# Performance work log

Hardware: AMD Instinct MI355X
Metric: run time of the kernel (lower is better)

## Reference

```python
import jax, jax.numpy as jnp
import numpy as np

# bior3.5 analysis filters (pywt conventions, dec_len = 12).
# dec_lo derived from the CDF(3,5) construction: sqrt(2)/2048 * conv([1,5,10,10,5,1], [-20,160,-524,832,-524,160,-20])
# matches pywt: [-0.0138107, 0.0414420, 0.0524806, -0.2679272, -0.0718155, 0.9667476, ...] (symmetric)
_DEC_LO = jnp.asarray(
    np.array([-20., 60., 76., -388., -104., 1400., 1400., -104., -388., 76., 60., -20.]) * np.sqrt(2.0) / 2048.0,
    dtype=jnp.float32)
# dec_hi = QMF of rec_lo = sqrt(2)*[1,3,3,1]/8, zero-padded to length 12 as pywt stores it (phase matters for periodization)
_DEC_HI = jnp.asarray(
    np.array([0., 0., 0., 0., -1., 3., -3., 1., 0., 0., 0., 0.]) * np.sqrt(2.0) / 8.0,
    dtype=jnp.float32)


def _dwt_last(x, f):
    # pywt mode='periodization' along last axis: out[i] = sum_j f[j] * x[(2i+1-j) mod N], N even -> length N//2.
    # Equivalent to wrap-padding F-2 on the left, then stride-2 valid correlation with reversed filter.
    F = f.shape[0]
    N = x.shape[-1]
    xp = jnp.concatenate([x[..., N - (F - 2):], x], axis=-1)  # [..., N+F-2]
    lhs = xp.reshape(-1, 1, xp.shape[-1])
    rhs = f[::-1].astype(x.dtype).reshape(1, 1, F)
    out = jax.lax.conv_general_dilated(lhs, rhs, window_strides=(2,), padding='VALID')  # [M,1,N//2]
    return out.reshape(*x.shape[:-1], N // 2)


def _dwt_axis(x, f, axis):
    x = jnp.swapaxes(x, axis, -1)
    return jnp.swapaxes(_dwt_last(x, f), axis, -1)


def _dwt2(x):
    # separable 2D DWT over the last two axes; pywt dwt2 keys: 'aa','da','ad','dd' (first letter = axis -2)
    lo = _dwt_axis(x, _DEC_LO, -1)
    hi = _dwt_axis(x, _DEC_HI, -1)
    aa = _dwt_axis(lo, _DEC_LO, -2)  # cA
    da = _dwt_axis(lo, _DEC_HI, -2)  # cH
    ad = _dwt_axis(hi, _DEC_LO, -2)  # cV
    dd = _dwt_axis(hi, _DEC_HI, -2)  # cD
    return aa, (da, ad, dd)


def _forward(x, k):
    # wavedec2 to level k; the torch module stacks 3 channels (we carry them as a batch-like dim)
    # and concatenates (cH, cV, cD) along dim 0 for each level, coarsest level first.
    a = x
    highs = []
    for _ in range(k):
        a, (da, ad, dd) = _dwt2(a)
        highs.insert(0, jnp.concatenate([da, ad, dd], axis=0))  # [3B, 3, h, w]
    return (a, *highs)


def setup_inputs() -> dict:
    key = jax.random.key(0)
    x = jax.random.normal(key, (8, 3, 1024, 1024), dtype=jnp.float32)
    return {"x": x, "k": 3}


def reference(x, k):
    return _forward(x, k)
```

## Files before the change

kernel.cpp:

```cpp
#include <hip/hip_runtime.h>


#define OW 32
#define OHS 16
#define NSTEP 4
#define ROWS_PB (OHS * NSTEP)
#define IN_ROWS 42
#define QPR 20
#define NQ (IN_ROWS * QPR)
#define SPITCH 84
#define TRS 42

template <int N>
__global__ __launch_bounds__(256, 4) void dwt2_level(
    const float* __restrict__ src,
    float* __restrict__ aa, float* __restrict__ da,
    float* __restrict__ ad, float* __restrict__ dd)
{
    constexpr float SQ2 = 1.41421356237309504880f;
    constexpr float c_lo[12] = {
        -20.f * SQ2 / 2048.f,  60.f * SQ2 / 2048.f,   76.f * SQ2 / 2048.f,
        -388.f * SQ2 / 2048.f, -104.f * SQ2 / 2048.f, 1400.f * SQ2 / 2048.f,
        1400.f * SQ2 / 2048.f, -104.f * SQ2 / 2048.f, -388.f * SQ2 / 2048.f,
        76.f * SQ2 / 2048.f,   60.f * SQ2 / 2048.f,   -20.f * SQ2 / 2048.f };
    constexpr float c_hi4[4] = { -SQ2 / 8.f, 3.f * SQ2 / 8.f, -3.f * SQ2 / 8.f, SQ2 / 8.f };

    constexpr int h    = N >> 1;
    constexpr int mask = N - 1;

    const int bc  = blockIdx.z;
    const int j0  = blockIdx.x * OW;
    const int i0  = blockIdx.y * ROWS_PB;
    const int tid = threadIdx.x;

    __shared__ float s_in[IN_ROWS * SPITCH];
    __shared__ float s_loT[OW * TRS];
    __shared__ float s_hiT[OW * TRS];

    const float* img = src + (unsigned)bc * (unsigned)(N * N);
    const int c0 = 2 * j0 - 12;

    auto ldq = [&](int s, int q) -> float4 {
        const int r  = q / QPR;
        const int c4 = q - r * QPR;
        const int gr = (2 * (i0 + OHS * s) - 10 + r) & mask;
        const int gc = (c0 + 4 * c4) & mask;
        return *(const float4*)(img + (unsigned)(gr * N + gc));
    };
    auto stq = [&](int q, float4 v) {
        const int r  = q / QPR;
        const int c4 = q - r * QPR;
        *(float4*)&s_in[r * SPITCH + 4 * c4] = v;
    };

    const bool has4 = tid < (NQ - 768);

    float4 pf0 = ldq(0, tid);
    float4 pf1 = ldq(0, tid + 256);
    float4 pf2 = ldq(0, tid + 512);
    float4 pf3 = make_float4(0.f, 0.f, 0.f, 0.f);
    if (has4) pf3 = ldq(0, tid + 768);
    stq(tid, pf0);
    stq(tid + 256, pf1);
    stq(tid + 512, pf2);
    if (has4) stq(tid + 768, pf3);

    for (int s = 0; s < NSTEP; ++s) {
        __syncthreads();

        if (s + 1 < NSTEP) {
            pf0 = ldq(s + 1, tid);
            pf1 = ldq(s + 1, tid + 256);
            pf2 = ldq(s + 1, tid + 512);
            if (has4) pf3 = ldq(s + 1, tid + 768);
        }

        if (tid < IN_ROWS * (OW / 8)) {
            const int m = tid & 3;
            const int r = tid >> 2;
            const float* p = &s_in[r * SPITCH + 16 * m];
            float v[28];
            #pragma unroll
            for (int q = 0; q < 7; ++q)
                *(float4*)&v[4 * q] = *(const float4*)&p[4 * q];
            #pragma unroll
            for (int d = 0; d < 8; ++d) {
                float lo = 0.f, hi = 0.f;
                #pragma unroll
                for (int jc = 0; jc < 12; ++jc)
                    lo += c_lo[jc] * v[2 * d + 13 - jc];
                #pragma unroll
                for (int k = 0; k < 4; ++k)
                    hi += c_hi4[k] * v[2 * d + 9 - k];
                s_loT[(8 * m + d) * TRS + r] = lo;
                s_hiT[(8 * m + d) * TRS + r] = hi;
            }
        }
        __syncthreads();

        {
            const int tx = tid & 31;
            const int ty = tid >> 5;
            float l[14], hh[14];
            #pragma unroll
            for (int e = 0; e < 7; ++e) {
                *(float2*)&l[2 * e]  = *(const float2*)&s_loT[tx * TRS + 4 * ty + 2 * e];
                *(float2*)&hh[2 * e] = *(const float2*)&s_hiT[tx * TRS + 4 * ty + 2 * e];
            }
            float vaa0 = 0.f, vaa1 = 0.f, vad0 = 0.f, vad1 = 0.f;
            #pragma unroll
            for (int jr = 0; jr < 12; ++jr) {
                vaa0 += c_lo[jr] * l[11 - jr];
                vaa1 += c_lo[jr] * l[13 - jr];
                vad0 += c_lo[jr] * hh[11 - jr];
                vad1 += c_lo[jr] * hh[13 - jr];
            }
            float vda0 = 0.f, vda1 = 0.f, vdd0 = 0.f, vdd1 = 0.f;
            #pragma unroll
            for (int k = 0; k < 4; ++k) {
                vda0 += c_hi4[k] * l[7 - k];
                vda1 += c_hi4[k] * l[9 - k];
                vdd0 += c_hi4[k] * hh[7 - k];
                vdd1 += c_hi4[k] * hh[9 - k];
            }
            const int orow = i0 + OHS * s + 2 * ty;
            const unsigned ob = (unsigned)((bc * h + orow) * h + j0 + tx);
            aa[ob] = vaa0;  aa[ob + h] = vaa1;
            da[ob] = vda0;  da[ob + h] = vda1;
            ad[ob] = vad0;  ad[ob + h] = vad1;
            dd[ob] = vdd0;  dd[ob + h] = vdd1;
        }

        if (s + 1 < NSTEP) {
            stq(tid, pf0);
            stq(tid + 256, pf1);
            stq(tid + 512, pf2);
            if (has4) stq(tid + 768, pf3);
        }
    }
}

extern "C" void kernel_launch(void* const* d_in, const int* in_sizes, int n_in,
                              void* d_out, int out_size, void* d_ws, size_t ws_size,
                              hipStream_t stream) {
    const float* x = (const float*)d_in[0];
    float* out = (float*)d_out;
    float* ws  = (float*)d_ws;

    const size_t s512 = (size_t)24 * 512 * 512;
    const size_t s256 = (size_t)24 * 256 * 256;
    const size_t s128 = (size_t)24 * 128 * 128;

    float* a_out = out;
    float* h3 = out + s128;
    float* h2 = out + 4 * s128;
    float* h1 = out + 4 * s128 + 3 * s256;

    float* aa1 = ws;
    float* aa2 = ws + s512;
    (void)in_sizes; (void)n_in; (void)out_size; (void)ws_size;

    dim3 blk(256, 1, 1);
    dwt2_level<1024><<<dim3(512 / OW, 512 / ROWS_PB, 24), blk, 0, stream>>>(
        x, aa1, h1, h1 + s512, h1 + 2 * s512);
    dwt2_level<512><<<dim3(256 / OW, 256 / ROWS_PB, 24), blk, 0, stream>>>(
        aa1, aa2, h2, h2 + s256, h2 + 2 * s256);
    dwt2_level<256><<<dim3(128 / OW, 128 / ROWS_PB, 24), blk, 0, stream>>>(
        aa2, a_out, h3, h3 + s128, h3 + 2 * s128);
}
```

Before: 76.06 us.

## Warp-specialize DWT block into loader and compute halves

Splits the 256-thread block so threads 128-255 only prefetch the next input tile (7 float4 each) and write it to shared memory, while threads 0-127 run the vertical filter pass with 4 outputs per thread. The shared transpose pitch changes from 42 to 43 to avoid bank conflicts, and launch bounds ask for 6 blocks per CU. The aim is to overlap global loads with compute and raise occupancy. In exchange, half the threads do the vertical pass with more work each and hold more registers (7 float4 buffers), and the unaligned pitch turns the vertical loads into scalar reads.

```diff
diff --git a/kernel.cpp b/kernel.cpp
--- a/kernel.cpp
+++ b/kernel.cpp
@@ -9,10 +9,10 @@
 #define QPR 20
 #define NQ (IN_ROWS * QPR)
 #define SPITCH 84
-#define TRS 42
+#define TRS 43
 
 template <int N>
-__global__ __launch_bounds__(256, 4) void dwt2_level(
+__global__ __launch_bounds__(256, 6) void dwt2_level(
     const float* __restrict__ src,
     float* __restrict__ aa, float* __restrict__ da,
     float* __restrict__ ad, float* __restrict__ dd)
@@ -53,29 +53,35 @@
         *(float4*)&s_in[r * SPITCH + 4 * c4] = v;
     };
 
-    const bool has4 = tid < (NQ - 768);
+    const bool loader = tid >= 128;
+    const int  lt     = tid - 128;
 
-    float4 pf0 = ldq(0, tid);
-    float4 pf1 = ldq(0, tid + 256);
-    float4 pf2 = ldq(0, tid + 512);
-    float4 pf3 = make_float4(0.f, 0.f, 0.f, 0.f);
-    if (has4) pf3 = ldq(0, tid + 768);
-    stq(tid, pf0);
-    stq(tid + 256, pf1);
-    stq(tid + 512, pf2);
-    if (has4) stq(tid + 768, pf3);
+    float4 pf[7];
+    if (loader) {
+        #pragma unroll
+        for (int k = 0; k < 7; ++k) {
+            const int q = lt + 128 * k;
+            if (q < NQ) pf[k] = ldq(0, q);
+        }
+        #pragma unroll
+        for (int k = 0; k < 7; ++k) {
+            const int q = lt + 128 * k;
+            if (q < NQ) stq(q, pf[k]);
+        }
+    }
 
     for (int s = 0; s < NSTEP; ++s) {
         __syncthreads();
 
-        if (s + 1 < NSTEP) {
-            pf0 = ldq(s + 1, tid);
-            pf1 = ldq(s + 1, tid + 256);
-            pf2 = ldq(s + 1, tid + 512);
-            if (has4) pf3 = ldq(s + 1, tid + 768);
+        if (loader && (s + 1 < NSTEP)) {
+            #pragma unroll
+            for (int k = 0; k < 7; ++k) {
+                const int q = lt + 128 * k;
+                if (q < NQ) pf[k] = ldq(s + 1, q);
+            }
         }
 
-        if (tid < IN_ROWS * (OW / 8)) {
+        if (tid < IN_ROWS * 4) {
             const int m = tid & 3;
             const int r = tid >> 2;
             const float* p = &s_in[r * SPITCH + 16 * m];
@@ -98,44 +104,42 @@
         }
         __syncthreads();
 
-        {
+        if (!loader) {
             const int tx = tid & 31;
-            const int ty = tid >> 5;
-            float l[14], hh[14];
+            const int g  = tid >> 5;
+            float l[18], hh[18];
             #pragma unroll
-            for (int e = 0; e < 7; ++e) {
-                *(float2*)&l[2 * e]  = *(const float2*)&s_loT[tx * TRS + 4 * ty + 2 * e];
-                *(float2*)&hh[2 * e] = *(const float2*)&s_hiT[tx * TRS + 4 * ty + 2 * e];
+            for (int e = 0; e < 18; ++e) {
+                l[e]  = s_loT[tx * TRS + 8 * g + e];
+                hh[e] = s_hiT[tx * TRS + 8 * g + e];
             }
-            float vaa0 = 0.f, vaa1 = 0.f, vad0 = 0.f, vad1 = 0.f;
             #pragma unroll
-            for (int jr = 0; jr < 12; ++jr) {
-                vaa0 += c_lo[jr] * l[11 - jr];
-                vaa1 += c_lo[jr] * l[13 - jr];
-                vad0 += c_lo[jr] * hh[11 - jr];
-                vad1 += c_lo[jr] * hh[13 - jr];
+            for (int u = 0; u < 4; ++u) {
+                float vaa = 0.f, vad = 0.f;
+                #pragma unroll
+                for (int jr = 0; jr < 12; ++jr) {
+                    vaa += c_lo[jr] * l[2 * u + 11 - jr];
+                    vad += c_lo[jr] * hh[2 * u + 11 - jr];
+                }
+                float vda = 0.f, vdd = 0.f;
+                #pragma unroll
+                for (int k = 0; k < 4; ++k) {
+                    vda += c_hi4[k] * l[2 * u + 7 - k];
+                    vdd += c_hi4[k] * hh[2 * u + 7 - k];
+                }
+                const int orow = i0 + OHS * s + 4 * g + u;
+                const unsigned ob = (unsigned)((bc * h + orow) * h + j0 + tx);
+                aa[ob] = vaa;
+                da[ob] = vda;
+                ad[ob] = vad;
+                dd[ob] = vdd;
             }
-            float vda0 = 0.f, vda1 = 0.f, vdd0 = 0.f, vdd1 = 0.f;
+        } else if (s + 1 < NSTEP) {
             #pragma unroll
-            for (int k = 0; k < 4; ++k) {
-                vda0 += c_hi4[k] * l[7 - k];
-                vda1 += c_hi4[k] * l[9 - k];
-                vdd0 += c_hi4[k] * hh[7 - k];
-                vdd1 += c_hi4[k] * hh[9 - k];
+            for (int k = 0; k < 7; ++k) {
+                const int q = lt + 128 * k;
+                if (q < NQ) stq(q, pf[k]);
             }
-            const int orow = i0 + OHS * s + 2 * ty;
-            const unsigned ob = (unsigned)((bc * h + orow) * h + j0 + tx);
-            aa[ob] = vaa0;  aa[ob + h] = vaa1;
-            da[ob] = vda0;  da[ob + h] = vda1;
-            ad[ob] = vad0;  ad[ob + h] = vad1;
-            dd[ob] = vdd0;  dd[ob + h] = vdd1;
-        }
-
-        if (s + 1 < NSTEP) {
-            stq(tid, pf0);
-            stq(tid + 256, pf1);
-            stq(tid + 512, pf2);
-            if (has4) stq(tid + 768, pf3);
         }
     }
 }
```

Result: slower. 110.2 us (+44.9%).

## Interleave lo/hi transpose buffer, use raw barriers, vary steps per level

Applied to the files above, without the earlier changes.

Merges the two transposed shared buffers into one interleaved float2 array, so each row pass does one 64-bit store and the column pass reads lo and hi together. Replaces __syncthreads with a raw LDS-wait plus s_barrier and scheduling fences, and moves the barrier to the end of each step. Makes the number of row steps per block a template parameter (4/2/1 for the three levels), giving the smaller levels more blocks and parallelism. Raises the launch-bounds occupancy hint from 4 to 5 blocks per CU. The manual barriers wait only on LDS counters and rely on the fences to keep the prefetch ordering correct.

```diff
diff --git a/kernel.cpp b/kernel.cpp
--- a/kernel.cpp
+++ b/kernel.cpp
@@ -3,16 +3,20 @@
 
 #define OW 32
 #define OHS 16
-#define NSTEP 4
-#define ROWS_PB (OHS * NSTEP)
 #define IN_ROWS 42
 #define QPR 20
-#define NQ (IN_ROWS * QPR)
+#define NQ 840
 #define SPITCH 84
-#define TRS 42
+#define PITCH 86
 
-template <int N>
-__global__ __launch_bounds__(256, 4) void dwt2_level(
+#define BAR() do { \
+    asm volatile("s_waitcnt lgkmcnt(0)" ::: "memory"); \
+    __builtin_amdgcn_s_barrier(); \
+    __builtin_amdgcn_sched_barrier(0); \
+  } while (0)
+
+template <int N, int NSTEP>
+__global__ __launch_bounds__(256, 5) void dwt2_level(
     const float* __restrict__ src,
     float* __restrict__ aa, float* __restrict__ da,
     float* __restrict__ ad, float* __restrict__ dd)
@@ -30,12 +34,11 @@
 
     const int bc  = blockIdx.z;
     const int j0  = blockIdx.x * OW;
-    const int i0  = blockIdx.y * ROWS_PB;
+    const int i0  = blockIdx.y * (OHS * NSTEP);
     const int tid = threadIdx.x;
 
     __shared__ float s_in[IN_ROWS * SPITCH];
-    __shared__ float s_loT[OW * TRS];
-    __shared__ float s_hiT[OW * TRS];
+    __shared__ float s_T[OW * PITCH];
 
     const float* img = src + (unsigned)bc * (unsigned)(N * N);
     const int c0 = 2 * j0 - 12;
@@ -64,18 +67,18 @@
     stq(tid + 256, pf1);
     stq(tid + 512, pf2);
     if (has4) stq(tid + 768, pf3);
+    BAR();
 
     for (int s = 0; s < NSTEP; ++s) {
-        __syncthreads();
-
         if (s + 1 < NSTEP) {
             pf0 = ldq(s + 1, tid);
             pf1 = ldq(s + 1, tid + 256);
             pf2 = ldq(s + 1, tid + 512);
             if (has4) pf3 = ldq(s + 1, tid + 768);
         }
+        __builtin_amdgcn_sched_barrier(0);
 
-        if (tid < IN_ROWS * (OW / 8)) {
+        if (tid < IN_ROWS * 4) {
             const int m = tid & 3;
             const int r = tid >> 2;
             const float* p = &s_in[r * SPITCH + 16 * m];
@@ -92,20 +95,20 @@
                 #pragma unroll
                 for (int k = 0; k < 4; ++k)
                     hi += c_hi4[k] * v[2 * d + 9 - k];
-                s_loT[(8 * m + d) * TRS + r] = lo;
-                s_hiT[(8 * m + d) * TRS + r] = hi;
+                *(float2*)&s_T[(8 * m + d) * PITCH + 2 * r] = make_float2(lo, hi);
             }
         }
-        __syncthreads();
+        BAR();
 
         {
             const int tx = tid & 31;
             const int ty = tid >> 5;
             float l[14], hh[14];
             #pragma unroll
-            for (int e = 0; e < 7; ++e) {
-                *(float2*)&l[2 * e]  = *(const float2*)&s_loT[tx * TRS + 4 * ty + 2 * e];
-                *(float2*)&hh[2 * e] = *(const float2*)&s_hiT[tx * TRS + 4 * ty + 2 * e];
+            for (int e = 0; e < 14; ++e) {
+                float2 p = *(const float2*)&s_T[tx * PITCH + 2 * (4 * ty + e)];
+                l[e]  = p.x;
+                hh[e] = p.y;
             }
             float vaa0 = 0.f, vaa1 = 0.f, vad0 = 0.f, vad1 = 0.f;
             #pragma unroll
@@ -137,6 +140,7 @@
             stq(tid + 512, pf2);
             if (has4) stq(tid + 768, pf3);
         }
+        BAR();
     }
 }
 
@@ -161,10 +165,10 @@
     (void)in_sizes; (void)n_in; (void)out_size; (void)ws_size;
 
     dim3 blk(256, 1, 1);
-    dwt2_level<1024><<<dim3(512 / OW, 512 / ROWS_PB, 24), blk, 0, stream>>>(
+    dwt2_level<1024, 4><<<dim3(16, 8, 24), blk, 0, stream>>>(
         x, aa1, h1, h1 + s512, h1 + 2 * s512);
-    dwt2_level<512><<<dim3(256 / OW, 256 / ROWS_PB, 24), blk, 0, stream>>>(
+    dwt2_level<512, 2><<<dim3(8, 8, 24), blk, 0, stream>>>(
         aa1, aa2, h2, h2 + s256, h2 + 2 * s256);
-    dwt2_level<256><<<dim3(128 / OW, 128 / ROWS_PB, 24), blk, 0, stream>>>(
+    dwt2_level<256, 1><<<dim3(4, 8, 24), blk, 0, stream>>>(
         aa2, a_out, h3, h3 + s128, h3 + 2 * s128);
 }
```

Measured after the change: 77.16 us. About the same (+1.4%).
